# Performance work log

Measured on AMD Instinct MI355X. Metric: run time of the kernel, lower is better.

The kernel has to match this reference:

```python
import jax, jax.numpy as jnp
import numpy as np

N, T, D, M = 16, 4096, 256, 512


def setup_inputs() -> dict:
    key = jax.random.key(0)
    k1, k2 = jax.random.split(key)
    x = jax.random.normal(k1, (N, T, D), dtype=jnp.float32)
    # codebook initialized like the module: uniform(-1/M, 1/M) then row-normalized
    init_bound = 1.0 / M
    emb = jax.random.uniform(k2, (M, D), dtype=jnp.float32, minval=-init_bound, maxval=init_bound)
    emb = emb / (jnp.linalg.norm(emb, axis=1, keepdims=True) + 1e-4)
    return {"x": x, "embedding": emb}


def reference(x, embedding):
    sg = jax.lax.stop_gradient
    # L2_distance: distances computed against the row-normalized codebook,
    # but the gather uses the raw (unnormalized) codebook.
    emb_norm = embedding / (jnp.linalg.norm(embedding, axis=1, keepdims=True) + 1e-4)
    x_flat = sg(x).reshape(-1, D)  # (N*T, D), detached in torch
    distances = (jnp.sum(emb_norm ** 2, axis=1)[None, :]
                 + jnp.sum(x_flat ** 2, axis=1, keepdims=True)
                 - 2.0 * (x_flat @ emb_norm.T))  # (N*T, M)
    indices = jnp.argmin(distances, axis=-1)  # (N*T,)
    encodings = jax.nn.one_hot(indices, M, dtype=jnp.float32)  # (N*T, M)
    quantized = embedding[indices].reshape(x.shape)  # (N, T, D)

    commitment_loss = jnp.mean((sg(x) - quantized) ** 2)
    quantized_ = x + sg(quantized - x)           # straight-through
    quantized_ = (quantized_ + quantized) / 2.0  # averaged with raw-grad path

    avg_probs = jnp.mean(encodings, axis=0)  # (M,)
    perplexity = jnp.exp(-jnp.sum(avg_probs * jnp.log(avg_probs + 1e-10)))
    return quantized_, commitment_loss, perplexity
```

## Files before the change

kernel.cpp:

```cpp
#include <hip/hip_runtime.h>
#include <hip/hip_bf16.h>


typedef _Float16 half8_t __attribute__((ext_vector_type(8)));
typedef _Float16 half4_t __attribute__((ext_vector_type(4)));
typedef float f32x4 __attribute__((ext_vector_type(4)));

static constexpr int kRows = 65536;
static constexpr int kD = 256;
static constexpr int kM = 512;
static constexpr int kBM = 128;

typedef const unsigned int __attribute__((address_space(1)))* gas_t;
typedef unsigned int __attribute__((address_space(3)))* las_t;

__global__ void vq_prep(const float* __restrict__ emb, _Float16* __restrict__ swz,
                        float* __restrict__ bias, unsigned int* __restrict__ hist,
                        float* __restrict__ loss) {
    const int j = blockIdx.x;
    const int lane = threadIdx.x;
    float4 v = ((const float4*)(emb + j * kD))[lane];
    float ss = v.x * v.x + v.y * v.y + v.z * v.z + v.w * v.w;
    #pragma unroll
    for (int off = 32; off > 0; off >>= 1) ss += __shfl_xor(ss, off);
    const float scale = 1.0f / (sqrtf(ss) + 1e-4f);
    if (lane == 0) bias[j] = 0.5f * ss * scale * scale;
    half4_t h;
    h[0] = (_Float16)(v.x * scale);
    h[1] = (_Float16)(v.y * scale);
    h[2] = (_Float16)(v.z * scale);
    h[3] = (_Float16)(v.w * scale);
    const int k0 = lane * 4;
    const int ko = k0 >> 5;
    const int qd = (k0 >> 3) & 3;
    const int jj = k0 & 7;
    const int off_h = (j >> 4) * 4096 + ko * 512 + (qd * 16 + (j & 15)) * 8 + jj;
    *(half4_t*)(swz + off_h) = h;
    if (j == 0) {
        for (int b = lane; b < kM; b += 64) hist[b] = 0u;
        if (lane == 0) loss[0] = 0.0f;
    }
}

__global__ __launch_bounds__(512, 4) void vq_main(
    const float* __restrict__ x, const float* __restrict__ emb,
    const _Float16* __restrict__ bswz, const float* __restrict__ bias,
    unsigned int* __restrict__ hist, float* __restrict__ loss_accum,
    float* __restrict__ out) {
    __shared__ _Float16 bb[128 * kD];
    __shared__ float lbias[kM];
    __shared__ unsigned int lhist[kM];
    __shared__ int lidx[kBM];
    __shared__ float lred[8];

    const int t = threadIdx.x;
    const int row0 = blockIdx.x * kBM;
    const int wave = t >> 6;
    const int lane = t & 63;
    const int qd = lane >> 4;
    const int ln = lane & 15;
    const int m0 = wave * 16;

    lhist[t] = 0u;
    lbias[t] = bias[t];

    half8_t a[8];
    {
        const float* xr = x + (size_t)(row0 + m0 + ln) * kD + qd * 8;
        #pragma unroll
        for (int ko = 0; ko < 8; ++ko) {
            const float4 v0 = *(const float4*)(xr + ko * 32);
            const float4 v1 = *(const float4*)(xr + ko * 32 + 4);
            half8_t h;
            h[0] = (_Float16)v0.x; h[1] = (_Float16)v0.y;
            h[2] = (_Float16)v0.z; h[3] = (_Float16)v0.w;
            h[4] = (_Float16)v1.x; h[5] = (_Float16)v1.y;
            h[6] = (_Float16)v1.z; h[7] = (_Float16)v1.w;
            a[ko] = h;
        }
    }

    float bv[4] = {-1e30f, -1e30f, -1e30f, -1e30f};
    int bi[4] = {0, 0, 0, 0};
    #pragma unroll 1
    for (int s = 0; s < 4; ++s) {
        __syncthreads();
        {
            const _Float16* src = bswz + (size_t)s * 32768 + t * 8;
            _Float16* dst = bb + t * 8;
            #pragma unroll
            for (int i = 0; i < 8; ++i)
                __builtin_amdgcn_global_load_lds((gas_t)(const void*)(src + i * 4096),
                                                 (las_t)(void*)(dst + i * 4096), 16, 0, 0);
        }
        __syncthreads();
        #pragma unroll
        for (int sub = 0; sub < 8; ++sub) {
            const int c = s * 128 + sub * 16 + ln;
            const float bbias = lbias[c];
            f32x4 acc = {-bbias, -bbias, -bbias, -bbias};
            const half8_t* bp = (const half8_t*)bb + sub * 512 + lane;
            #pragma unroll
            for (int ko = 0; ko < 8; ++ko)
                acc = __builtin_amdgcn_mfma_f32_16x16x32_f16(a[ko], bp[ko * 64], acc, 0, 0, 0);
            #pragma unroll
            for (int r = 0; r < 4; ++r)
                if (acc[r] > bv[r]) { bv[r] = acc[r]; bi[r] = c; }
        }
    }

    #pragma unroll
    for (int r = 0; r < 4; ++r) {
        #pragma unroll
        for (int off = 1; off < 16; off <<= 1) {
            const float ov = __shfl_xor(bv[r], off);
            const int oi = __shfl_xor(bi[r], off);
            if (ov > bv[r] || (ov == bv[r] && oi < bi[r])) { bv[r] = ov; bi[r] = oi; }
        }
        if (ln == 0) {
            const int row = m0 + qd * 4 + r;
            lidx[row] = bi[r];
            atomicAdd(&lhist[bi[r]], 1u);
        }
    }
    __syncthreads();

    float lsum = 0.0f;
    {
        const float* xg = x + (size_t)row0 * kD;
        float* og = out + (size_t)row0 * kD;
        #pragma unroll
        for (int i = 0; i < 16; ++i) {
            const int g = t * 4 + i * 2048;
            const int r = g >> 8;
            const float4 xv = *(const float4*)(xg + g);
            const int idx = lidx[r];
            const float4 q = *(const float4*)(emb + (size_t)idx * kD + (g & 255));
            const float d0 = xv.x - q.x, d1 = xv.y - q.y, d2 = xv.z - q.z, d3 = xv.w - q.w;
            lsum += d0 * d0 + d1 * d1 + d2 * d2 + d3 * d3;
            float4 o;
            o.x = ((xv.x + (q.x - xv.x)) + q.x) * 0.5f;
            o.y = ((xv.y + (q.y - xv.y)) + q.y) * 0.5f;
            o.z = ((xv.z + (q.z - xv.z)) + q.z) * 0.5f;
            o.w = ((xv.w + (q.w - xv.w)) + q.w) * 0.5f;
            *(float4*)&og[g] = o;
        }
    }
    #pragma unroll
    for (int off = 32; off > 0; off >>= 1) lsum += __shfl_xor(lsum, off);
    if (lane == 0) lred[wave] = lsum;
    __syncthreads();
    if (t == 0) {
        float bs = 0.f;
        #pragma unroll
        for (int w = 0; w < 8; ++w) bs += lred[w];
        atomicAdd(loss_accum, bs);
    }

    const unsigned int h0 = lhist[t];
    if (h0) atomicAdd(&hist[t], h0);
}

__global__ void vq_final(const unsigned int* __restrict__ hist,
                         const float* __restrict__ loss_accum,
                         float* __restrict__ out) {
    const int t = threadIdx.x;
    __shared__ float sr[4];
    float s = 0.0f;
    for (int b = t; b < kM; b += 256) {
        const float p = (float)hist[b] * (1.0f / 65536.0f);
        s += p * logf(p + 1e-10f);
    }
    #pragma unroll
    for (int off = 32; off > 0; off >>= 1) s += __shfl_xor(s, off);
    if ((t & 63) == 0) sr[t >> 6] = s;
    __syncthreads();
    if (t == 0) {
        const float tot = sr[0] + sr[1] + sr[2] + sr[3];
        out[16777217] = expf(-tot);
        out[16777216] = loss_accum[0] * (1.0f / 16777216.0f);
    }
}

extern "C" void kernel_launch(void* const* d_in, const int* in_sizes, int n_in,
                              void* d_out, int out_size, void* d_ws, size_t ws_size,
                              hipStream_t stream) {
    const float* x = (const float*)d_in[0];
    const float* emb = (const float*)d_in[1];
    char* ws = (char*)d_ws;
    _Float16* bswz = (_Float16*)ws;
    float* bias = (float*)(ws + 262144);
    unsigned int* hist = (unsigned int*)(ws + 262144 + 2048);
    float* loss = (float*)(ws + 262144 + 4096);
    float* out = (float*)d_out;

    vq_prep<<<kM, 64, 0, stream>>>(emb, bswz, bias, hist, loss);
    vq_main<<<kRows / kBM, 512, 0, stream>>>(x, emb, bswz, bias, hist, loss, out);
    vq_final<<<1, 256, 0, stream>>>(hist, loss, out);
}
```

Measured before the change: 139.3 us.

## Halve row tile, split codebook across waves, double-buffer codebook loads

Row tile per block drops from 128 to 64. The 8 waves now form 4 row groups times 2 codebook halves, so each wave pair splits the 16-column codebook sub-tiles and the two partial argmins are merged through shared memory. The codebook is streamed in 32-row chunks through two LDS buffers, so the next chunk's global-to-LDS load overlaps MFMA compute on the current one. LDS use drops from 64KB to 32KB for higher occupancy (launch bounds 8), at the cost of twice as many blocks, each reloading the full codebook, plus more barriers.

```diff
diff --git a/kernel.cpp b/kernel.cpp
--- a/kernel.cpp
+++ b/kernel.cpp
@@ -9,7 +9,7 @@
 static constexpr int kRows = 65536;
 static constexpr int kD = 256;
 static constexpr int kM = 512;
-static constexpr int kBM = 128;
+static constexpr int kBM = 64;
 
 typedef const unsigned int __attribute__((address_space(1)))* gas_t;
 typedef unsigned int __attribute__((address_space(3)))* las_t;
@@ -42,15 +42,18 @@
     }
 }
 
-__global__ __launch_bounds__(512, 4) void vq_main(
+__global__ __launch_bounds__(512, 8) void vq_main(
     const float* __restrict__ x, const float* __restrict__ emb,
     const _Float16* __restrict__ bswz, const float* __restrict__ bias,
     unsigned int* __restrict__ hist, float* __restrict__ loss_accum,
     float* __restrict__ out) {
-    __shared__ _Float16 bb[128 * kD];
+    __shared__ _Float16 bb0[32 * kD];
+    __shared__ _Float16 bb1[32 * kD];
     __shared__ float lbias[kM];
     __shared__ unsigned int lhist[kM];
     __shared__ int lidx[kBM];
+    __shared__ float lbv[kBM * 2];
+    __shared__ int lbi[kBM * 2];
     __shared__ float lred[8];
 
     const int t = threadIdx.x;
@@ -59,10 +62,19 @@
     const int lane = t & 63;
     const int qd = lane >> 4;
     const int ln = lane & 15;
-    const int m0 = wave * 16;
+    const int m0 = (wave & 3) * 16;
+    const int h = wave >> 2;
 
     lhist[t] = 0u;
     lbias[t] = bias[t];
+
+    {
+        const _Float16* src = bswz + t * 8;
+        __builtin_amdgcn_global_load_lds((gas_t)(const void*)(src),
+                                         (las_t)(void*)(bb0 + t * 8), 16, 0, 0);
+        __builtin_amdgcn_global_load_lds((gas_t)(const void*)(src + 4096),
+                                         (las_t)(void*)(bb0 + t * 8 + 4096), 16, 0, 0);
+    }
 
     half8_t a[8];
     {
@@ -71,42 +83,47 @@
         for (int ko = 0; ko < 8; ++ko) {
             const float4 v0 = *(const float4*)(xr + ko * 32);
             const float4 v1 = *(const float4*)(xr + ko * 32 + 4);
-            half8_t h;
-            h[0] = (_Float16)v0.x; h[1] = (_Float16)v0.y;
-            h[2] = (_Float16)v0.z; h[3] = (_Float16)v0.w;
-            h[4] = (_Float16)v1.x; h[5] = (_Float16)v1.y;
-            h[6] = (_Float16)v1.z; h[7] = (_Float16)v1.w;
-            a[ko] = h;
-        }
-    }
+            half8_t hh;
+            hh[0] = (_Float16)v0.x; hh[1] = (_Float16)v0.y;
+            hh[2] = (_Float16)v0.z; hh[3] = (_Float16)v0.w;
+            hh[4] = (_Float16)v1.x; hh[5] = (_Float16)v1.y;
+            hh[6] = (_Float16)v1.z; hh[7] = (_Float16)v1.w;
+            a[ko] = hh;
+        }
+    }
+    __syncthreads();
 
     float bv[4] = {-1e30f, -1e30f, -1e30f, -1e30f};
     int bi[4] = {0, 0, 0, 0};
+
+    auto issue = [&](int s, _Float16* dst) {
+        const _Float16* src = bswz + (size_t)s * 8192 + t * 8;
+        __builtin_amdgcn_global_load_lds((gas_t)(const void*)(src),
+                                         (las_t)(void*)(dst + t * 8), 16, 0, 0);
+        __builtin_amdgcn_global_load_lds((gas_t)(const void*)(src + 4096),
+                                         (las_t)(void*)(dst + t * 8 + 4096), 16, 0, 0);
+    };
+    auto compute = [&](int s, const _Float16* buf) {
+        const int c = s * 32 + h * 16 + ln;
+        const float bbias = lbias[c];
+        f32x4 acc = {-bbias, -bbias, -bbias, -bbias};
+        const half8_t* bp = (const half8_t*)buf + h * 512 + lane;
+        #pragma unroll
+        for (int ko = 0; ko < 8; ++ko)
+            acc = __builtin_amdgcn_mfma_f32_16x16x32_f16(a[ko], bp[ko * 64], acc, 0, 0, 0);
+        #pragma unroll
+        for (int r = 0; r < 4; ++r)
+            if (acc[r] > bv[r] || (acc[r] == bv[r] && c < bi[r])) { bv[r] = acc[r]; bi[r] = c; }
+    };
+
     #pragma unroll 1
-    for (int s = 0; s < 4; ++s) {
+    for (int s = 0; s < 16; s += 2) {
+        issue(s + 1, bb1);
+        compute(s, bb0);
         __syncthreads();
-        {
-            const _Float16* src = bswz + (size_t)s * 32768 + t * 8;
-            _Float16* dst = bb + t * 8;
-            #pragma unroll
-            for (int i = 0; i < 8; ++i)
-                __builtin_amdgcn_global_load_lds((gas_t)(const void*)(src + i * 4096),
-                                                 (las_t)(void*)(dst + i * 4096), 16, 0, 0);
-        }
+        if (s + 2 < 16) issue(s + 2, bb0);
+        compute(s + 1, bb1);
         __syncthreads();
-        #pragma unroll
-        for (int sub = 0; sub < 8; ++sub) {
-            const int c = s * 128 + sub * 16 + ln;
-            const float bbias = lbias[c];
-            f32x4 acc = {-bbias, -bbias, -bbias, -bbias};
-            const half8_t* bp = (const half8_t*)bb + sub * 512 + lane;
-            #pragma unroll
-            for (int ko = 0; ko < 8; ++ko)
-                acc = __builtin_amdgcn_mfma_f32_16x16x32_f16(a[ko], bp[ko * 64], acc, 0, 0, 0);
-            #pragma unroll
-            for (int r = 0; r < 4; ++r)
-                if (acc[r] > bv[r]) { bv[r] = acc[r]; bi[r] = c; }
-        }
     }
 
     #pragma unroll
@@ -119,9 +136,17 @@
         }
         if (ln == 0) {
             const int row = m0 + qd * 4 + r;
-            lidx[row] = bi[r];
-            atomicAdd(&lhist[bi[r]], 1u);
-        }
+            lbv[row * 2 + h] = bv[r];
+            lbi[row * 2 + h] = bi[r];
+        }
+    }
+    __syncthreads();
+    if (t < kBM) {
+        const float v0 = lbv[t * 2], v1 = lbv[t * 2 + 1];
+        const int i0 = lbi[t * 2], i1 = lbi[t * 2 + 1];
+        const int win = (v1 > v0 || (v1 == v0 && i1 < i0)) ? i1 : i0;
+        lidx[t] = win;
+        atomicAdd(&lhist[win], 1u);
     }
     __syncthreads();
 
@@ -130,7 +155,7 @@
         const float* xg = x + (size_t)row0 * kD;
         float* og = out + (size_t)row0 * kD;
         #pragma unroll
-        for (int i = 0; i < 16; ++i) {
+        for (int i = 0; i < 8; ++i) {
             const int g = t * 4 + i * 2048;
             const int r = g >> 8;
             const float4 xv = *(const float4*)(xg + g);
```

Result: slower. 144.9 us (+4.1%).

## Stream codebook from global into registers, two row tiles per wave, algebraic loss

Applied to the files above, without the earlier changes.

The LDS-staged codebook is replaced by per-wave register double-buffering of swizzled codebook fragments loaded straight from global/L2. Each wave now handles 32 rows, so every B fragment feeds two MFMA tiles, and the block shrinks to 256 threads. The commitment loss is computed algebraically from ||x||^2, precomputed per-code constants and the winning dot product, so the epilogue no longer rereads x and only gathers and writes codebook rows. The trade-offs are more global/L2 traffic for the codebook, higher register pressure, and a loss that now depends on the fp16 dot-product value rather than exact fp32 differences.

```diff
diff --git a/kernel.cpp b/kernel.cpp
--- a/kernel.cpp
+++ b/kernel.cpp
@@ -1,5 +1,4 @@
 #include <hip/hip_runtime.h>
-#include <hip/hip_bf16.h>
 
 
 typedef _Float16 half8_t __attribute__((ext_vector_type(8)));
@@ -11,20 +10,22 @@
 static constexpr int kM = 512;
 static constexpr int kBM = 128;
 
-typedef const unsigned int __attribute__((address_space(1)))* gas_t;
-typedef unsigned int __attribute__((address_space(3)))* las_t;
-
 __global__ void vq_prep(const float* __restrict__ emb, _Float16* __restrict__ swz,
-                        float* __restrict__ bias, unsigned int* __restrict__ hist,
-                        float* __restrict__ loss) {
+                        float* __restrict__ bias, float2* __restrict__ cab,
+                        unsigned int* __restrict__ hist, float* __restrict__ loss) {
     const int j = blockIdx.x;
     const int lane = threadIdx.x;
     float4 v = ((const float4*)(emb + j * kD))[lane];
     float ss = v.x * v.x + v.y * v.y + v.z * v.z + v.w * v.w;
     #pragma unroll
     for (int off = 32; off > 0; off >>= 1) ss += __shfl_xor(ss, off);
-    const float scale = 1.0f / (sqrtf(ss) + 1e-4f);
-    if (lane == 0) bias[j] = 0.5f * ss * scale * scale;
+    const float s = sqrtf(ss) + 1e-4f;
+    const float scale = 1.0f / s;
+    if (lane == 0) {
+        bias[j] = 0.5f * ss * scale * scale;
+        cab[j] = make_float2(ss * (1.0f - scale),
+                             -2.0f * s);
+    }
     half4_t h;
     h[0] = (_Float16)(v.x * scale);
     h[1] = (_Float16)(v.y * scale);
@@ -42,123 +43,162 @@
     }
 }
 
-__global__ __launch_bounds__(512, 4) void vq_main(
+__global__ __launch_bounds__(256, 2) void vq_main(
     const float* __restrict__ x, const float* __restrict__ emb,
     const _Float16* __restrict__ bswz, const float* __restrict__ bias,
+    const float2* __restrict__ cab,
     unsigned int* __restrict__ hist, float* __restrict__ loss_accum,
     float* __restrict__ out) {
-    __shared__ _Float16 bb[128 * kD];
-    __shared__ float lbias[kM];
     __shared__ unsigned int lhist[kM];
     __shared__ int lidx[kBM];
-    __shared__ float lred[8];
+    __shared__ float lred[16];
 
     const int t = threadIdx.x;
-    const int row0 = blockIdx.x * kBM;
     const int wave = t >> 6;
     const int lane = t & 63;
+    const int ln = lane & 15;
     const int qd = lane >> 4;
-    const int ln = lane & 15;
-    const int m0 = wave * 16;
+    const int r0 = blockIdx.x * kBM + wave * 32;
 
     lhist[t] = 0u;
-    lbias[t] = bias[t];
-
-    half8_t a[8];
+    lhist[t + 256] = 0u;
+    __syncthreads();
+
+    half8_t ba[8], bb[8];
     {
-        const float* xr = x + (size_t)(row0 + m0 + ln) * kD + qd * 8;
+        const _Float16* b0 = bswz + lane * 8;
+        #pragma unroll
+        for (int ko = 0; ko < 8; ++ko) ba[ko] = *(const half8_t*)(b0 + ko * 512);
+    }
+    float bias_c = bias[ln];
+
+    half8_t a0[8], a1[8];
+    float ssq0 = 0.0f, ssq1 = 0.0f;
+    {
+        const float* xr0 = x + (size_t)(r0 + ln) * kD + qd * 8;
+        const float* xr1 = xr0 + 16 * kD;
         #pragma unroll
         for (int ko = 0; ko < 8; ++ko) {
-            const float4 v0 = *(const float4*)(xr + ko * 32);
-            const float4 v1 = *(const float4*)(xr + ko * 32 + 4);
-            half8_t h;
-            h[0] = (_Float16)v0.x; h[1] = (_Float16)v0.y;
-            h[2] = (_Float16)v0.z; h[3] = (_Float16)v0.w;
-            h[4] = (_Float16)v1.x; h[5] = (_Float16)v1.y;
-            h[6] = (_Float16)v1.z; h[7] = (_Float16)v1.w;
-            a[ko] = h;
-        }
-    }
-
-    float bv[4] = {-1e30f, -1e30f, -1e30f, -1e30f};
-    int bi[4] = {0, 0, 0, 0};
+            const float4 u0 = *(const float4*)(xr0 + ko * 32);
+            const float4 u1 = *(const float4*)(xr0 + ko * 32 + 4);
+            const float4 w0 = *(const float4*)(xr1 + ko * 32);
+            const float4 w1 = *(const float4*)(xr1 + ko * 32 + 4);
+            half8_t h0, h1;
+            h0[0] = (_Float16)u0.x; h0[1] = (_Float16)u0.y;
+            h0[2] = (_Float16)u0.z; h0[3] = (_Float16)u0.w;
+            h0[4] = (_Float16)u1.x; h0[5] = (_Float16)u1.y;
+            h0[6] = (_Float16)u1.z; h0[7] = (_Float16)u1.w;
+            h1[0] = (_Float16)w0.x; h1[1] = (_Float16)w0.y;
+            h1[2] = (_Float16)w0.z; h1[3] = (_Float16)w0.w;
+            h1[4] = (_Float16)w1.x; h1[5] = (_Float16)w1.y;
+            h1[6] = (_Float16)w1.z; h1[7] = (_Float16)w1.w;
+            a0[ko] = h0; a1[ko] = h1;
+            ssq0 += u0.x*u0.x + u0.y*u0.y + u0.z*u0.z + u0.w*u0.w
+                  + u1.x*u1.x + u1.y*u1.y + u1.z*u1.z + u1.w*u1.w;
+            ssq1 += w0.x*w0.x + w0.y*w0.y + w0.z*w0.z + w0.w*w0.w
+                  + w1.x*w1.x + w1.y*w1.y + w1.z*w1.z + w1.w*w1.w;
+        }
+    }
+    ssq0 += __shfl_xor(ssq0, 16); ssq0 += __shfl_xor(ssq0, 32);
+    ssq1 += __shfl_xor(ssq1, 16); ssq1 += __shfl_xor(ssq1, 32);
+
+    float bv0[4] = {-1e30f, -1e30f, -1e30f, -1e30f};
+    float bv1[4] = {-1e30f, -1e30f, -1e30f, -1e30f};
+    int bi0[4] = {0, 0, 0, 0};
+    int bi1[4] = {0, 0, 0, 0};
+
+    auto compute = [&](int g, const half8_t (&b)[8], float bg) {
+        f32x4 acc0 = {-bg, -bg, -bg, -bg};
+        f32x4 acc1 = {-bg, -bg, -bg, -bg};
+        #pragma unroll
+        for (int ko = 0; ko < 8; ++ko) {
+            acc0 = __builtin_amdgcn_mfma_f32_16x16x32_f16(a0[ko], b[ko], acc0, 0, 0, 0);
+            acc1 = __builtin_amdgcn_mfma_f32_16x16x32_f16(a1[ko], b[ko], acc1, 0, 0, 0);
+        }
+        const int c = g * 16 + ln;
+        #pragma unroll
+        for (int r = 0; r < 4; ++r) {
+            if (acc0[r] > bv0[r]) { bv0[r] = acc0[r]; bi0[r] = c; }
+            if (acc1[r] > bv1[r]) { bv1[r] = acc1[r]; bi1[r] = c; }
+        }
+    };
+
     #pragma unroll 1
-    for (int s = 0; s < 4; ++s) {
-        __syncthreads();
+    for (int g = 0; g < 32; g += 2) {
         {
-            const _Float16* src = bswz + (size_t)s * 32768 + t * 8;
-            _Float16* dst = bb + t * 8;
+            const _Float16* bn = bswz + (g + 1) * 4096 + lane * 8;
             #pragma unroll
-            for (int i = 0; i < 8; ++i)
-                __builtin_amdgcn_global_load_lds((gas_t)(const void*)(src + i * 4096),
-                                                 (las_t)(void*)(dst + i * 4096), 16, 0, 0);
-        }
-        __syncthreads();
-        #pragma unroll
-        for (int sub = 0; sub < 8; ++sub) {
-            const int c = s * 128 + sub * 16 + ln;
-            const float bbias = lbias[c];
-            f32x4 acc = {-bbias, -bbias, -bbias, -bbias};
-            const half8_t* bp = (const half8_t*)bb + sub * 512 + lane;
+            for (int ko = 0; ko < 8; ++ko) bb[ko] = *(const half8_t*)(bn + ko * 512);
+        }
+        const float bias_n = bias[(g + 1) * 16 + ln];
+        compute(g, ba, bias_c);
+        if (g + 2 < 32) {
+            const _Float16* bn = bswz + (g + 2) * 4096 + lane * 8;
             #pragma unroll
-            for (int ko = 0; ko < 8; ++ko)
-                acc = __builtin_amdgcn_mfma_f32_16x16x32_f16(a[ko], bp[ko * 64], acc, 0, 0, 0);
-            #pragma unroll
-            for (int r = 0; r < 4; ++r)
-                if (acc[r] > bv[r]) { bv[r] = acc[r]; bi[r] = c; }
-        }
+            for (int ko = 0; ko < 8; ++ko) ba[ko] = *(const half8_t*)(bn + ko * 512);
+            bias_c = bias[(g + 2) * 16 + ln];
+        }
+        compute(g + 1, bb, bias_n);
     }
 
     #pragma unroll
     for (int r = 0; r < 4; ++r) {
         #pragma unroll
         for (int off = 1; off < 16; off <<= 1) {
-            const float ov = __shfl_xor(bv[r], off);
-            const int oi = __shfl_xor(bi[r], off);
-            if (ov > bv[r] || (ov == bv[r] && oi < bi[r])) { bv[r] = ov; bi[r] = oi; }
-        }
-        if (ln == 0) {
-            const int row = m0 + qd * 4 + r;
-            lidx[row] = bi[r];
-            atomicAdd(&lhist[bi[r]], 1u);
-        }
-    }
-    __syncthreads();
+            const float ov0 = __shfl_xor(bv0[r], off);
+            const int   oi0 = __shfl_xor(bi0[r], off);
+            if (ov0 > bv0[r] || (ov0 == bv0[r] && oi0 < bi0[r])) { bv0[r] = ov0; bi0[r] = oi0; }
+            const float ov1 = __shfl_xor(bv1[r], off);
+            const int   oi1 = __shfl_xor(bi1[r], off);
+            if (ov1 > bv1[r] || (ov1 == bv1[r] && oi1 < bi1[r])) { bv1[r] = ov1; bi1[r] = oi1; }
+        }
+    }
+
+    float ssA[4], ssB[4];
+    #pragma unroll
+    for (int r = 0; r < 4; ++r) {
+        ssA[r] = __shfl(ssq0, qd * 4 + r);
+        ssB[r] = __shfl(ssq1, qd * 4 + r);
+    }
 
     float lsum = 0.0f;
+    if (ln == 0) {
+        #pragma unroll
+        for (int r = 0; r < 4; ++r) {
+            const int row = qd * 4 + r;
+            const float2 c0 = cab[bi0[r]];
+            lidx[wave * 32 + row] = bi0[r];
+            atomicAdd(&lhist[bi0[r]], 1u);
+            lsum += ssA[r] + c0.x + c0.y * bv0[r];
+            const float2 c1 = cab[bi1[r]];
+            lidx[wave * 32 + 16 + row] = bi1[r];
+            atomicAdd(&lhist[bi1[r]], 1u);
+            lsum += ssB[r] + c1.x + c1.y * bv1[r];
+        }
+        lred[wave * 4 + qd] = lsum;
+    }
+
     {
-        const float* xg = x + (size_t)row0 * kD;
-        float* og = out + (size_t)row0 * kD;
-        #pragma unroll
-        for (int i = 0; i < 16; ++i) {
-            const int g = t * 4 + i * 2048;
-            const int r = g >> 8;
-            const float4 xv = *(const float4*)(xg + g);
-            const int idx = lidx[r];
-            const float4 q = *(const float4*)(emb + (size_t)idx * kD + (g & 255));
-            const float d0 = xv.x - q.x, d1 = xv.y - q.y, d2 = xv.z - q.z, d3 = xv.w - q.w;
-            lsum += d0 * d0 + d1 * d1 + d2 * d2 + d3 * d3;
-            float4 o;
-            o.x = ((xv.x + (q.x - xv.x)) + q.x) * 0.5f;
-            o.y = ((xv.y + (q.y - xv.y)) + q.y) * 0.5f;
-            o.z = ((xv.z + (q.z - xv.z)) + q.z) * 0.5f;
-            o.w = ((xv.w + (q.w - xv.w)) + q.w) * 0.5f;
-            *(float4*)&og[g] = o;
-        }
-    }
-    #pragma unroll
-    for (int off = 32; off > 0; off >>= 1) lsum += __shfl_xor(lsum, off);
-    if (lane == 0) lred[wave] = lsum;
+        float* og = out + (size_t)r0 * kD;
+        #pragma unroll 4
+        for (int i = 0; i < 32; ++i) {
+            const int idx = lidx[wave * 32 + i];
+            const float4 q = *(const float4*)(emb + (size_t)idx * kD + lane * 4);
+            *(float4*)(og + i * kD + lane * 4) = q;
+        }
+    }
+
     __syncthreads();
     if (t == 0) {
         float bs = 0.f;
         #pragma unroll
-        for (int w = 0; w < 8; ++w) bs += lred[w];
+        for (int w = 0; w < 16; ++w) bs += lred[w];
         atomicAdd(loss_accum, bs);
     }
-
     const unsigned int h0 = lhist[t];
     if (h0) atomicAdd(&hist[t], h0);
+    const unsigned int h1 = lhist[t + 256];
+    if (h1) atomicAdd(&hist[t + 256], h1);
 }
 
 __global__ void vq_final(const unsigned int* __restrict__ hist,
@@ -192,9 +232,10 @@
     float* bias = (float*)(ws + 262144);
     unsigned int* hist = (unsigned int*)(ws + 262144 + 2048);
     float* loss = (float*)(ws + 262144 + 4096);
+    float2* cab = (float2*)(ws + 262144 + 4096 + 16);
     float* out = (float*)d_out;
 
-    vq_prep<<<kM, 64, 0, stream>>>(emb, bswz, bias, hist, loss);
-    vq_main<<<kRows / kBM, 512, 0, stream>>>(x, emb, bswz, bias, hist, loss, out);
+    vq_prep<<<kM, 64, 0, stream>>>(emb, bswz, bias, cab, hist, loss);
+    vq_main<<<kRows / kBM, 256, 0, stream>>>(x, emb, bswz, bias, cab, hist, loss, out);
     vq_final<<<1, 256, 0, stream>>>(hist, loss, out);
 }
```

Result: slower. 151.7 us (+8.9%).
